# Kernel optimization log

Measured on AMD Instinct MI355X. Metric: run time of the kernel, lower is better.

The kernel has to match this reference:

```python
import jax, jax.numpy as jnp
import numpy as np
import math

H = 1024      # hidden_size
NH = 16       # num_attention_heads
HD = H // NH  # head_dim = 64
FF = 4096     # intermediate_size
AD = 256      # adapter_hidden_size
NB = 320      # num_buckets
MAXD = 800    # max_bucket_distance
B = 4
S = 1024
EPS = 1e-5


def _rel_bucket(rel):
    # HF WavLM _relative_positions_bucket
    nb = NB // 2
    buckets = (rel > 0).astype(jnp.int32) * nb
    rel = jnp.abs(rel)
    max_exact = nb // 2
    is_small = rel < max_exact
    large = max_exact + (
        jnp.log(jnp.maximum(rel, 1).astype(jnp.float32) / max_exact)
        / math.log(MAXD / max_exact) * (nb - max_exact)
    ).astype(jnp.int32)
    large = jnp.minimum(large, nb - 1)
    return buckets + jnp.where(is_small, rel, large)


def _ln(x, g, b):
    m = x.mean(-1, keepdims=True)
    v = ((x - m) ** 2).mean(-1, keepdims=True)
    return (x - m) * jax.lax.rsqrt(v + EPS) * g + b


def setup_inputs() -> dict:
    key = jax.random.key(0)
    ks = jax.random.split(key, 12)
    sc = 0.02
    w = lambda k, shape: jax.random.normal(k, shape, jnp.float32) * sc
    return dict(
        x=jax.random.normal(ks[0], (B, S, H), jnp.float32),
        Wq=w(ks[1], (H, H)), bq=jnp.zeros((H,), jnp.float32),
        Wk=w(ks[2], (H, H)), bk=jnp.zeros((H,), jnp.float32),
        Wv=w(ks[3], (H, H)), bv=jnp.zeros((H,), jnp.float32),
        Wo=w(ks[4], (H, H)), bo=jnp.zeros((H,), jnp.float32),
        Wg=w(ks[5], (8, HD)), bg=jnp.zeros((8,), jnp.float32),
        gru_const=jnp.ones((1, NH, 1, 1), jnp.float32),
        rel_embed=w(ks[6], (NB, NH)),
        ln1_g=jnp.ones((H,), jnp.float32), ln1_b=jnp.zeros((H,), jnp.float32),
        W1=w(ks[7], (FF, H)), b1=jnp.zeros((FF,), jnp.float32),
        W2=w(ks[8], (H, FF)), b2=jnp.zeros((H,), jnp.float32),
        ln2_g=jnp.ones((H,), jnp.float32), ln2_b=jnp.zeros((H,), jnp.float32),
        Wad=w(ks[9], (AD, H)), bad=jnp.zeros((AD,), jnp.float32),
        Wau=w(ks[10], (H, AD)), bau=jnp.zeros((H,), jnp.float32),
    )


def reference(x, Wq, bq, Wk, bk, Wv, bv, Wo, bo, Wg, bg, gru_const, rel_embed,
              ln1_g, ln1_b, W1, b1, W2, b2, ln2_g, ln2_b, Wad, bad, Wau, bau):
    b, s, _ = x.shape
    # --- relative position bias (first layer: position_bias=None) ---
    pos = jnp.arange(s)
    rel = pos[None, :] - pos[:, None]                 # memory - context
    pos_bias = rel_embed[_rel_bucket(rel)].transpose(2, 0, 1)  # (nh, s, s)

    # --- GRU-style gating of the bias (per batch, head, query pos) ---
    xh = x.reshape(b, s, NH, HD).transpose(0, 2, 1, 3)         # (b, nh, s, hd)
    gproj = jnp.einsum('bhsd,ed->bhse', xh, Wg) + bg           # (b, nh, s, 8)
    gproj = gproj.reshape(b, NH, s, 2, 4).sum(-1)              # (b, nh, s, 2)
    gate = jax.nn.sigmoid(gproj)
    gate_a, gate_b = gate[..., 0:1], gate[..., 1:2]            # (b, nh, s, 1)
    gate_out = gate_a * (gate_b * gru_const - 1.0) + 2.0       # (b, nh, s, 1)
    gated_bias = gate_out * pos_bias[None]                     # (b, nh, s, s)

    # --- multi-head self-attention with additive gated bias ---
    q = (x @ Wq.T + bq).reshape(b, s, NH, HD)
    k = (x @ Wk.T + bk).reshape(b, s, NH, HD)
    v = (x @ Wv.T + bv).reshape(b, s, NH, HD)
    scores = jnp.einsum('bihd,bjhd->bhij', q, k) * (HD ** -0.5) + gated_bias
    attn = jax.nn.softmax(scores, axis=-1)
    ctx = jnp.einsum('bhij,bjhd->bihd', attn, v).reshape(b, s, H)
    attn_out = ctx @ Wo.T + bo

    # --- residual + LN, FFN + adapter (idx_without_adapter=None path) + LN ---
    h = _ln(x + attn_out, ln1_g, ln1_b)
    ff = jax.nn.gelu(h @ W1.T + b1, approximate=False) @ W2.T + b2
    adapt = jax.nn.elu(h @ Wad.T + bad) @ Wau.T + bau
    h = h + ff + adapt
    return _ln(h, ln2_g, ln2_b)
```

## Files before the change

### kernel.cpp

```cpp
#include <hip/hip_runtime.h>
#include <cmath>

typedef unsigned short u16;
using short8 = __attribute__((ext_vector_type(8))) short;
using f32x4  = __attribute__((ext_vector_type(4))) float;

__device__ __forceinline__ u16 f2bf(float f) {
  union { float f; unsigned u; } c; c.f = f;
  unsigned r = c.u + 0x7fffu + ((c.u >> 16) & 1u);
  return (u16)(r >> 16);
}
__device__ __forceinline__ float bf2f(u16 b) {
  union { unsigned u; float f; } c; c.u = ((unsigned)b) << 16;
  return c.f;
}

__device__ __forceinline__ void gld_lds16(void* lds, const void* g) {
  __builtin_amdgcn_global_load_lds(
      (const __attribute__((address_space(1))) void*)g,
      (__attribute__((address_space(3))) void*)lds, 16, 0, 0);
}

__device__ __forceinline__ float gelu_fast(float t) {
  float u = 0.7978845608f * t * (1.f + 0.044715f * t * t);
  float th = 1.f - 2.f / (__expf(2.f * u) + 1.f);
  return 0.5f * t * (1.f + th);
}

__global__ __launch_bounds__(256) void cvt_bf16(const float* __restrict__ in,
                                                u16* __restrict__ out, int n4) {
  int i = blockIdx.x * 256 + threadIdx.x;
  if (i >= n4) return;
  float4 v = ((const float4*)in)[i];
  ushort4 o;
  o.x = f2bf(v.x); o.y = f2bf(v.y); o.z = f2bf(v.z); o.w = f2bf(v.w);
  ((ushort4*)out)[i] = o;
}

__global__ __launch_bounds__(256) void cvt_pad(const float* __restrict__ in,
                                               u16* __restrict__ out,
                                               int incols4, int outstride, int n4) {
  int i = blockIdx.x * 256 + threadIdx.x;
  if (i >= n4) return;
  int row = i / incols4, c = i - row * incols4;
  float4 v = ((const float4*)in)[i];
  ushort4 o;
  o.x = f2bf(v.x); o.y = f2bf(v.y); o.z = f2bf(v.z); o.w = f2bf(v.w);
  *(ushort4*)&out[(size_t)row * outstride + c * 4] = o;
}

__global__ __launch_bounds__(256) void btab_kernel(const float* __restrict__ rel_embed,
                                                   float* __restrict__ btab) {
  int idx = blockIdx.x * 256 + threadIdx.x;
  if (idx >= 16 * 2048) return;
  int h = idx >> 11;
  int d = idx & 2047;
  if (d >= 2047) return;
  int rel = d - 1023;
  int bucket = (rel > 0) ? 160 : 0;
  int ar = rel < 0 ? -rel : rel;
  if (ar < 80) {
    bucket += ar;
  } else {
    int large = 80 + (int)(logf((float)ar / 80.0f) / 2.3025851f * 80.0f);
    if (large > 159) large = 159;
    bucket += large;
  }
  btab[h * 2048 + d] = rel_embed[bucket * 16 + h];
}

__global__ __launch_bounds__(256) void gate_kernel(const float* __restrict__ x,
                                                   const float* __restrict__ Wg,
                                                   const float* __restrict__ bg,
                                                   const float* __restrict__ gc,
                                                   float* __restrict__ gate_out) {
  int gw = blockIdx.x * 4 + (threadIdx.x >> 6);
  int lane = threadIdx.x & 63;
  int s = gw & 1023, bh = gw >> 10, b = bh >> 4, h = bh & 15;
  float wA = Wg[lane] + Wg[64 + lane] + Wg[128 + lane] + Wg[192 + lane];
  float wB = Wg[256 + lane] + Wg[320 + lane] + Wg[384 + lane] + Wg[448 + lane];
  float xv = x[((size_t)(b * 1024 + s)) * 1024 + h * 64 + lane];
  float pa = xv * wA, pb = xv * wB;
  #pragma unroll
  for (int m = 1; m < 64; m <<= 1) {
    pa += __shfl_xor(pa, m, 64);
    pb += __shfl_xor(pb, m, 64);
  }
  if (lane == 0) {
    float bgA = bg[0] + bg[1] + bg[2] + bg[3];
    float bgB = bg[4] + bg[5] + bg[6] + bg[7];
    float ga = 1.f / (1.f + expf(-(pa + bgA)));
    float gb = 1.f / (1.f + expf(-(pb + bgB)));
    gate_out[(size_t)bh * 1024 + s] = ga * (gb * gc[h] - 1.f) + 2.f;
  }
}

__global__ __launch_bounds__(256) void vtrans_kernel(const u16* __restrict__ vb,
                                                     u16* __restrict__ vt) {
  __shared__ u16 tile[64 * 65];
  int bh = blockIdx.y, b = bh >> 4, h = bh & 15;
  int s0 = blockIdx.x * 64;
  int tid = threadIdx.x;
  int r = tid >> 3, c = (tid & 7) * 8;
  #pragma unroll
  for (int p = 0; p < 2; ++p) {
    int s = p * 32 + r;
    uint4 vv = *(const uint4*)&vb[((size_t)(b * 1024 + s0 + s)) * 1024 + h * 64 + c];
    const u16* pv = (const u16*)&vv;
    #pragma unroll
    for (int e = 0; e < 8; ++e) tile[(c + e) * 65 + s] = pv[e];
  }
  __syncthreads();
  int d = tid & 63, jc0 = tid >> 6;
  #pragma unroll
  for (int jc = jc0; jc < 8; jc += 4) {
    u16 tmp[8];
    #pragma unroll
    for (int e = 0; e < 8; ++e) tmp[e] = tile[d * 65 + jc * 8 + e];
    *(uint4*)&vt[((size_t)(bh * 64 + d)) * 1024 + s0 + jc * 8] = *(uint4*)tmp;
  }
}

#define VMCNT(n) asm volatile("s_waitcnt vmcnt(" #n ")" ::: "memory")

#define G256_LDA(BUF, KK, MH)                                               \
  af_[0] = *(const short8*)&lds[BUF][0][KK][aBase + (MH) * 2048 + 0];       \
  af_[1] = *(const short8*)&lds[BUF][0][KK][aBase + (MH) * 2048 + 512];     \
  af_[2] = *(const short8*)&lds[BUF][0][KK][aBase + (MH) * 2048 + 1024];    \
  af_[3] = *(const short8*)&lds[BUF][0][KK][aBase + (MH) * 2048 + 1536];
#define G256_LDB(BUF, KK)                                                   \
  bf_[0] = *(const short8*)&lds[BUF][1][KK][bBase + 0];                     \
  bf_[1] = *(const short8*)&lds[BUF][1][KK][bBase + 512];                   \
  bf_[2] = *(const short8*)&lds[BUF][1][KK][bBase + 1024];                  \
  bf_[3] = *(const short8*)&lds[BUF][1][KK][bBase + 1536];
#define G256_MFMA(MH)                                                       \
  _Pragma("unroll") for (int mi = 0; mi < 4; ++mi)                          \
  _Pragma("unroll") for (int ni = 0; ni < 4; ++ni)                          \
    acc[(MH) * 4 + mi][ni] = __builtin_amdgcn_mfma_f32_16x16x32_bf16(       \
        af_[mi], bf_[ni], acc[(MH) * 4 + mi][ni], 0, 0, 0);
#define G256_TILE(BUF)                                                      \
  G256_LDB(BUF, 0)                                                          \
  G256_LDA(BUF, 0, 0)                                                       \
  G256_MFMA(0)                                                              \
  G256_LDA(BUF, 0, 1)                                                       \
  G256_MFMA(1)                                                              \
  G256_LDB(BUF, 1)                                                          \
  G256_LDA(BUF, 1, 0)                                                       \
  G256_MFMA(0)                                                              \
  G256_LDA(BUF, 1, 1)                                                       \
  G256_MFMA(1)

template <int MODE>
__global__ __launch_bounds__(512, 2) void gemm256(
    const u16* __restrict__ A, const u16* __restrict__ Bw,
    int lda, int ldb, int kt_hi, int kt_lo, int z_hi,
    const float* __restrict__ bias0, const float* __restrict__ bias1,
    const float* __restrict__ bias2,
    float* __restrict__ outf, float* __restrict__ outf2,
    float* __restrict__ outf3, int ldo,
    u16* __restrict__ ob0, u16* __restrict__ ob1, u16* __restrict__ ob2) {
  __shared__ __align__(16) u16 lds[2][2][2][8192];

  const int tid = threadIdx.x;
  const int lane = tid & 63, wave = tid >> 6;
  const int quad = lane >> 4, l16 = lane & 15;
  const int wm = wave >> 2, wn = wave & 3;

  const int gx = gridDim.x, gy = gridDim.y;
  int flat = blockIdx.x + gx * (blockIdx.y + gy * blockIdx.z);
  const int cpx = (gx * gy * gridDim.z) >> 3;
  flat = (flat & 7) * cpx + (flat >> 3);
  const int bmi = flat % gx;
  int rest = flat / gx;
  const int bni = rest % gy;
  const int kz = rest / gy;

  const int bm = bmi * 256, bn = bni * 256;
  const int nkt = (kz < z_hi) ? kt_hi : kt_lo;
  const int ktb = (kz < z_hi) ? kz * kt_hi : z_hi * kt_hi + (kz - z_hi) * kt_lo;

  const int srow = wave * 16 + (lane >> 2);
  const int sk = (((lane & 3) ^ ((lane >> 3) & 3)) << 3);
  const u16* aG = A + (size_t)(bm + srow) * lda + (size_t)ktb * 64 + sk;
  const u16* bG = Bw + (size_t)(bn + srow) * ldb + (size_t)ktb * 64 + sk;
  const size_t aS = (size_t)128 * lda, bS = (size_t)128 * ldb;

  const int xsw = ((quad ^ ((l16 >> 1) & 3)) << 3);
  const int aBase = (wm * 128 + l16) * 32 + xsw;
  const int bBase = (wn * 64 + l16) * 32 + xsw;

  auto stA = [&](int buf, int kh, int kt) {
    const u16* g = aG + kt * 64 + kh * 32;
    u16* d = (u16*)&lds[buf][0][kh][wave * 512];
    gld_lds16(d, g);
    gld_lds16(d + 4096, g + aS);
  };
  auto stB = [&](int buf, int kh, int kt) {
    const u16* g = bG + kt * 64 + kh * 32;
    u16* d = (u16*)&lds[buf][1][kh][wave * 512];
    gld_lds16(d, g);
    gld_lds16(d + 4096, g + bS);
  };

  f32x4 acc[8][4] = {};
  short8 af_[4], bf_[4];

  stA(0, 0, 0); stB(0, 0, 0); stA(0, 1, 0); stB(0, 1, 0);
  VMCNT(0);
  __builtin_amdgcn_s_barrier();

  for (int J = 0; J < (nkt >> 1); ++J) {
    {
      const int t1 = 2 * J + 1;
      stA(1, 0, t1); stB(1, 0, t1); stA(1, 1, t1); stB(1, 1, t1);
      G256_TILE(0)
      VMCNT(0);
      __builtin_amdgcn_s_barrier();
    }
    {
      const int t2 = 2 * J + 2;
      if (t2 < nkt) { stA(0, 0, t2); stB(0, 0, t2); stA(0, 1, t2); stB(0, 1, t2); }
      G256_TILE(1)
      VMCNT(0);
      __builtin_amdgcn_s_barrier();
    }
  }

  const int m0 = bm + wm * 128 + quad * 4;
  const int n0 = bn + wn * 64 + l16;

  if constexpr (MODE == 0) {
    const int seg = bn >> 10;
    const float* bs = seg == 0 ? bias0 : (seg == 1 ? bias1 : bias2);
    u16* dst = seg == 0 ? ob0 : (seg == 1 ? ob1 : ob2);
    const float sc = seg == 0 ? 0.125f : 1.0f;
    const int nb = (bn & 1023) + wn * 64 + l16;
    #pragma unroll
    for (int a = 0; a < 8; ++a)
      #pragma unroll
      for (int ni = 0; ni < 4; ++ni) {
        int nn = nb + ni * 16;
        float bv = bs[nn];
        #pragma unroll
        for (int r = 0; r < 4; ++r) {
          int m = m0 + a * 16 + r;
          dst[(size_t)m * 1024 + nn] = f2bf((acc[a][ni][r] + bv) * sc);
        }
      }
  } else if constexpr (MODE == 2) {
    const bool is_gelu = (bn < 4096);
    #pragma unroll
    for (int a = 0; a < 8; ++a)
      #pragma unroll
      for (int ni = 0; ni < 4; ++ni) {
        int nn = n0 + ni * 16;
        float bv = is_gelu ? bias0[nn] : bias1[nn - 4096];
        #pragma unroll
        for (int r = 0; r < 4; ++r) {
          int m = m0 + a * 16 + r;
          float t = acc[a][ni][r] + bv;
          float res;
          if (is_gelu) res = gelu_fast(t);
          else         res = t > 0.f ? t : (__expf(t) - 1.f);
          ob0[(size_t)m * 4352 + nn] = f2bf(res);
        }
      }
  } else {
    float* op = (kz == 0) ? outf
              : (kz == 1) ? outf + 4194304
              : (kz == 2) ? outf2 : outf3;
    #pragma unroll
    for (int a = 0; a < 8; ++a)
      #pragma unroll
      for (int ni = 0; ni < 4; ++ni) {
        int nn = n0 + ni * 16;
        #pragma unroll
        for (int r = 0; r < 4; ++r)
          op[(size_t)(m0 + a * 16 + r) * ldo + nn] = acc[a][ni][r];
      }
  }
}

__global__ __launch_bounds__(256, 2) void attn_kernel(
    const u16* __restrict__ qb, const u16* __restrict__ kb, const u16* __restrict__ vt,
    const float* __restrict__ gate, const float* __restrict__ btab,
    u16* __restrict__ ctxb) {
  __shared__ __align__(16) u16 Ps[4][16 * 64];
  __shared__ u16 btl[2048];
  __shared__ float gbuf[64];

  const int tid = threadIdx.x;
  const int lane = tid & 63, wave = tid >> 6;
  const int quad = lane >> 4, l16 = lane & 15;
  const int bh = blockIdx.x, b = bh >> 4, h = bh & 15;
  const int it0 = blockIdx.y * 64;

  for (int idx = tid; idx < 2047; idx += 256) btl[idx] = f2bf(btab[h * 2048 + idx]);
  if (tid < 64) gbuf[tid] = gate[(size_t)bh * 1024 + it0 + tid];

  short8 aq[2];
  #pragma unroll
  for (int c = 0; c < 2; ++c)
    aq[c] = *(const short8*)&qb[((size_t)(b * 1024 + it0 + wave * 16 + l16)) * 1024 +
                                h * 64 + c * 32 + quad * 8];

  short8 kA[2][4], kB[2][4];
  auto loadK = [&](short8 (&kr)[2][4], int jt) {
    const int j0 = jt * 64;
    #pragma unroll
    for (int c = 0; c < 2; ++c)
      #pragma unroll
      for (int nt = 0; nt < 4; ++nt)
        kr[c][nt] = *(const short8*)&kb[((size_t)(b * 1024 + j0 + nt * 16 + l16)) * 1024 +
                                        h * 64 + c * 32 + quad * 8];
  };
  loadK(kA, 0);

  f32x4 oacc[4] = {};
  float mrow[4], lrow[4];
  #pragma unroll
  for (int r = 0; r < 4; ++r) { mrow[r] = -1e30f; lrow[r] = 0.f; }

  __syncthreads();

  auto body = [&](int jt, short8 (&kc)[2][4], short8 (&kn)[2][4], bool pf) {
    const int j0 = jt * 64;
    if (pf) loadK(kn, jt + 1);

    f32x4 sacc[4] = {};
    #pragma unroll
    for (int c = 0; c < 2; ++c)
      #pragma unroll
      for (int nt = 0; nt < 4; ++nt)
        sacc[nt] = __builtin_amdgcn_mfma_f32_16x16x32_bf16(aq[c], kc[c][nt], sacc[nt], 0, 0, 0);

    short8 bv[2][4];
    #pragma unroll
    for (int c = 0; c < 2; ++c)
      #pragma unroll
      for (int dt = 0; dt < 4; ++dt)
        bv[c][dt] = *(const short8*)&vt[((size_t)(bh * 64 + dt * 16 + l16)) * 1024 +
                                        j0 + c * 32 + quad * 8];

    float sc[4][4], mt[4];
    #pragma unroll
    for (int r = 0; r < 4; ++r) {
      int i_loc = wave * 16 + quad * 4 + r;
      int i_glob = it0 + i_loc;
      float g = gbuf[i_loc];
      float mx = -1e30f;
      #pragma unroll
      for (int nt = 0; nt < 4; ++nt) {
        int j = j0 + nt * 16 + l16;
        float s = sacc[nt][r] + g * bf2f(btl[j - i_glob + 1023]);
        sc[nt][r] = s;
        mx = fmaxf(mx, s);
      }
      mt[r] = mx;
    }
    #pragma unroll
    for (int m = 1; m < 16; m <<= 1)
      #pragma unroll
      for (int r = 0; r < 4; ++r) mt[r] = fmaxf(mt[r], __shfl_xor(mt[r], m, 64));

    float alpha[4], ls[4];
    #pragma unroll
    for (int r = 0; r < 4; ++r) {
      float mnew = fmaxf(mrow[r], mt[r]);
      alpha[r] = __expf(mrow[r] - mnew);
      mrow[r] = mnew;
      float lsum = 0.f;
      #pragma unroll
      for (int nt = 0; nt < 4; ++nt) {
        float p = __expf(sc[nt][r] - mnew);
        sc[nt][r] = p;
        lsum += p;
      }
      ls[r] = lsum;
    }
    #pragma unroll
    for (int m = 1; m < 16; m <<= 1)
      #pragma unroll
      for (int r = 0; r < 4; ++r) ls[r] += __shfl_xor(ls[r], m, 64);
    #pragma unroll
    for (int r = 0; r < 4; ++r) lrow[r] = lrow[r] * alpha[r] + ls[r];

    #pragma unroll
    for (int nt = 0; nt < 4; ++nt)
      #pragma unroll
      for (int r = 0; r < 4; ++r)
        Ps[wave][(nt * 2 + (l16 >> 3)) * 128 + (quad * 4 + r) * 8 + (l16 & 7)] = f2bf(sc[nt][r]);

    #pragma unroll
    for (int dt = 0; dt < 4; ++dt)
      #pragma unroll
      for (int r = 0; r < 4; ++r) oacc[dt][r] *= alpha[r];

    #pragma unroll
    for (int c = 0; c < 2; ++c) {
      short8 ap = *(const short8*)&Ps[wave][(c * 4 + quad) * 128 + l16 * 8];
      #pragma unroll
      for (int dt = 0; dt < 4; ++dt)
        oacc[dt] = __builtin_amdgcn_mfma_f32_16x16x32_bf16(ap, bv[c][dt], oacc[dt], 0, 0, 0);
    }
  };

  for (int J = 0; J < 8; ++J) {
    body(2 * J,     kA, kB, true);
    body(2 * J + 1, kB, kA, J < 7);
  }

  #pragma unroll
  for (int dt = 0; dt < 4; ++dt)
    #pragma unroll
    for (int r = 0; r < 4; ++r) {
      int i_loc = wave * 16 + quad * 4 + r;
      int d = dt * 16 + l16;
      float o = oacc[dt][r] / lrow[r];
      ctxb[((size_t)(b * 1024 + it0 + i_loc)) * 1024 + h * 64 + d] = f2bf(o);
    }
}

template <bool WRITE_BF16, bool TWO_BIAS, int NP>
__global__ __launch_bounds__(256) void redln_kernel(
    const float* __restrict__ p0, const float* __restrict__ p1,
    const float* __restrict__ p2, const float* __restrict__ p3,
    const float* __restrict__ extra, const float* __restrict__ bias,
    const float* __restrict__ bias2,
    const float* __restrict__ g, const float* __restrict__ bta,
    float* __restrict__ outf, u16* __restrict__ outb) {
  __shared__ float red[8];
  int row = blockIdx.x, tid = threadIdx.x;
  int lane = tid & 63, wave = tid >> 6;
  size_t base = (size_t)row * 1024 + tid * 4;
  float4 a = *(const float4*)&p0[base];
  float4 bb = *(const float4*)&p1[base];
  float4 c = *(const float4*)&extra[base];
  float4 d = *(const float4*)&bias[tid * 4];
  float4 v;
  v.x = a.x + bb.x + c.x + d.x;
  v.y = a.y + bb.y + c.y + d.y;
  v.z = a.z + bb.z + c.z + d.z;
  v.w = a.w + bb.w + c.w + d.w;
  if (NP == 4) {
    float4 e2 = *(const float4*)&p2[base];
    float4 e3 = *(const float4*)&p3[base];
    v.x += e2.x + e3.x; v.y += e2.y + e3.y;
    v.z += e2.z + e3.z; v.w += e2.w + e3.w;
  }
  if (TWO_BIAS) {
    float4 d2 = *(const float4*)&bias2[tid * 4];
    v.x += d2.x; v.y += d2.y; v.z += d2.z; v.w += d2.w;
  }
  float s = v.x + v.y + v.z + v.w;
  #pragma unroll
  for (int m = 1; m < 64; m <<= 1) s += __shfl_xor(s, m, 64);
  if (lane == 0) red[wave] = s;
  __syncthreads();
  float mean = (red[0] + red[1] + red[2] + red[3]) * (1.f / 1024.f);
  float d0 = v.x - mean, d1 = v.y - mean, d2 = v.z - mean, d3 = v.w - mean;
  float sq = d0 * d0 + d1 * d1 + d2 * d2 + d3 * d3;
  #pragma unroll
  for (int m = 1; m < 64; m <<= 1) sq += __shfl_xor(sq, m, 64);
  if (lane == 0) red[4 + wave] = sq;
  __syncthreads();
  float var = (red[4] + red[5] + red[6] + red[7]) * (1.f / 1024.f);
  float rstd = rsqrtf(var + 1e-5f);
  float dd[4] = {d0, d1, d2, d3};
  #pragma unroll
  for (int e = 0; e < 4; ++e) {
    int cidx = tid * 4 + e;
    float val = dd[e] * rstd * g[cidx] + bta[cidx];
    outf[(size_t)row * 1024 + cidx] = val;
    if (WRITE_BF16) outb[(size_t)row * 1024 + cidx] = f2bf(val);
  }
}

extern "C" void kernel_launch(void* const* d_in, const int* in_sizes, int n_in,
                              void* d_out, int out_size, void* d_ws, size_t ws_size,
                              hipStream_t stream) {
  const float* x    = (const float*)d_in[0];
  const float* Wq   = (const float*)d_in[1];  const float* bq  = (const float*)d_in[2];
  const float* Wk   = (const float*)d_in[3];  const float* bk  = (const float*)d_in[4];
  const float* Wv   = (const float*)d_in[5];  const float* bv  = (const float*)d_in[6];
  const float* Wo   = (const float*)d_in[7];  const float* bo  = (const float*)d_in[8];
  const float* Wg   = (const float*)d_in[9];  const float* bg  = (const float*)d_in[10];
  const float* gc   = (const float*)d_in[11];
  const float* rel  = (const float*)d_in[12];
  const float* ln1g = (const float*)d_in[13]; const float* ln1b = (const float*)d_in[14];
  const float* W1   = (const float*)d_in[15]; const float* b1  = (const float*)d_in[16];
  const float* W2   = (const float*)d_in[17]; const float* b2  = (const float*)d_in[18];
  const float* ln2g = (const float*)d_in[19]; const float* ln2b = (const float*)d_in[20];
  const float* Wad  = (const float*)d_in[21]; const float* bad = (const float*)d_in[22];
  const float* Wau  = (const float*)d_in[23]; const float* bau = (const float*)d_in[24];
  float* out = (float*)d_out;

  char* ws = (char*)d_ws;
  const size_t MB = 1ull << 20;
  const size_t KB = 1ull << 10;
  (void)n_in; (void)in_sizes; (void)out_size;

  const bool big = ws_size >= (135ull << 20);

  u16 *xb, *wqkv, *qb, *kb, *vbp, *vtb, *ctxb, *wob, *w1ad, *w2au, *ffadp, *hb;
  float *gate, *btab, *P0, *P1, *P2, *P3, *hf;
  xb    = (u16*)(ws + 0 * MB);
  wqkv  = (u16*)(ws + 8 * MB);
  ffadp = (u16*)(ws + 0 * MB);
  P0    = (float*)(ws + 34 * MB);
  P1    = (float*)(ws + 50 * MB);
  float* PW2 = (float*)(ws + 0 * MB);
  float* PW3 = (float*)(ws + 16 * MB);
  if (big) {
    P2   = (float*)(ws + 66 * MB);
    P3   = (float*)(ws + 82 * MB);
    qb   = (u16*)(ws + 66 * MB);
    kb   = (u16*)(ws + 74 * MB);
    vbp  = (u16*)(ws + 82 * MB);
    vtb  = (u16*)(ws + 90 * MB);
    hb   = (u16*)(ws + 82 * MB);
    ctxb = (u16*)(ws + 98 * MB);
    hf   = (float*)(ws + 98 * MB);
    wob  = (u16*)(ws + 114 * MB);
    w1ad = (u16*)(ws + 116 * MB);
    w2au = (u16*)(ws + 125 * MB);
    gate = (float*)(ws + 133 * MB + 512 * KB);
    btab = (float*)(ws + 133 * MB + 768 * KB);
  } else {
    qb   = (u16*)(ws + 14 * MB);
    kb   = (u16*)(ws + 22 * MB);
    vbp  = (u16*)(ws + 30 * MB);
    vtb  = (u16*)(ws + 38 * MB);
    gate = (float*)(ws + 46 * MB);
    btab = (float*)(ws + 46 * MB + 256 * KB);
    ctxb = (u16*)(ws + 66 * MB);
    wob  = (u16*)(ws + 74 * MB);
    w1ad = (u16*)(ws + 76 * MB);
    w2au = (u16*)(ws + 85 * MB);
    hf   = (float*)(ws + 94 * MB);
    hb   = (u16*)(ws + 110 * MB);
    P2   = (float*)(ws + 66 * MB);
    P3   = (float*)(ws + 14 * MB);
  }

  auto cvt = [&](const float* src, u16* dst, int n) {
    cvt_bf16<<<(n / 4 + 255) / 256, 256, 0, stream>>>(src, dst, n / 4);
  };
  cvt(x, xb, 4096 * 1024);
  cvt(Wq, wqkv,               1024 * 1024);
  cvt(Wk, wqkv + 1024 * 1024, 1024 * 1024);
  cvt(Wv, wqkv + 2 * 1024 * 1024, 1024 * 1024);
  cvt(Wo, wob, 1024 * 1024);
  cvt(W1, w1ad, 4096 * 1024);
  cvt(Wad, w1ad + 4096 * 1024, 256 * 1024);
  cvt_pad<<<(1024 * 1024 + 255) / 256, 256, 0, stream>>>(W2, w2au, 1024, 4352, 1024 * 1024);
  cvt_pad<<<(64 * 1024 + 255) / 256, 256, 0, stream>>>(Wau, w2au + 4096, 64, 4352, 64 * 1024);

  btab_kernel<<<128, 256, 0, stream>>>(rel, btab);
  gate_kernel<<<16384, 256, 0, stream>>>(x, Wg, bg, gc, gate);

  gemm256<0><<<dim3(16, 12, 1), 512, 0, stream>>>(xb, wqkv, 1024, 1024, 16, 16, 1,
      bq, bk, bv, nullptr, nullptr, nullptr, 0, qb, kb, vbp);
  vtrans_kernel<<<dim3(16, 64), 256, 0, stream>>>(vbp, vtb);
  attn_kernel<<<dim3(64, 16), 256, 0, stream>>>(qb, kb, vtb, gate, btab, ctxb);
  gemm256<3><<<dim3(16, 4, 4), 512, 0, stream>>>(ctxb, wob, 1024, 1024, 4, 4, 4,
      nullptr, nullptr, nullptr, P0, PW2, PW3, 1024, nullptr, nullptr, nullptr);
  redln_kernel<true, false, 4><<<4096, 256, 0, stream>>>(P0, P1, PW2, PW3, x, bo, nullptr,
      ln1g, ln1b, hf, hb);
  gemm256<2><<<dim3(16, 17, 1), 512, 0, stream>>>(hb, w1ad, 1024, 1024, 16, 16, 1,
      b1, bad, nullptr, nullptr, nullptr, nullptr, 0, ffadp, nullptr, nullptr);
  gemm256<3><<<dim3(16, 4, 4), 512, 0, stream>>>(ffadp, w2au, 4352, 4352, 18, 16, 2,
      nullptr, nullptr, nullptr, P0, P2, P3, 1024, nullptr, nullptr, nullptr);
  redln_kernel<false, true, 4><<<4096, 256, 0, stream>>>(P0, P1, P2, P3, hf, b2, bau,
      ln2g, ln2b, out, nullptr);
}
```

Baseline: 531.5 us.

## Stage K/V tiles in double-buffered LDS via direct global-to-LDS loads

The attention kernel now has the four waves cooperatively copy each 64x64 K and V tile into double-buffered shared memory with global_load_lds. Each wave then reads its MFMA operands from LDS instead of loading full K and V tiles from global memory separately. This removes the fourfold redundant global traffic for K/V across waves, at the cost of a workgroup barrier every iteration and more LDS use. The occupancy hint of 2 blocks per CU is dropped.

```diff
diff --git a/kernel.cpp b/kernel.cpp
--- a/kernel.cpp
+++ b/kernel.cpp
@@ -281,10 +281,12 @@
   }
 }
 
-__global__ __launch_bounds__(256, 2) void attn_kernel(
+__global__ __launch_bounds__(256) void attn_kernel(
     const u16* __restrict__ qb, const u16* __restrict__ kb, const u16* __restrict__ vt,
     const float* __restrict__ gate, const float* __restrict__ btab,
     u16* __restrict__ ctxb) {
+  __shared__ __align__(16) u16 Ks[2][64 * 64];
+  __shared__ __align__(16) u16 Vs[2][64 * 64];
   __shared__ __align__(16) u16 Ps[4][16 * 64];
   __shared__ u16 btl[2048];
   __shared__ float gbuf[64];
@@ -294,6 +296,19 @@
   const int quad = lane >> 4, l16 = lane & 15;
   const int bh = blockIdx.x, b = bh >> 4, h = bh & 15;
   const int it0 = blockIdx.y * 64;
+  const int sr = lane & 15;
+  const int skc = (lane >> 4) * 8;
+
+  auto stage = [&](int buf, int jt) {
+    const int j0 = jt * 64;
+    #pragma unroll
+    for (int hf = 0; hf < 2; ++hf) {
+      gld_lds16(&Ks[buf][wave * 1024 + hf * 512],
+                &kb[((size_t)(b * 1024 + j0 + wave * 16 + sr)) * 1024 + h * 64 + hf * 32 + skc]);
+      gld_lds16(&Vs[buf][wave * 1024 + hf * 512],
+                &vt[((size_t)(bh * 64 + wave * 16 + sr)) * 1024 + j0 + hf * 32 + skc]);
+    }
+  };
 
   for (int idx = tid; idx < 2047; idx += 256) btl[idx] = f2bf(btab[h * 2048 + idx]);
   if (tid < 64) gbuf[tid] = gate[(size_t)bh * 1024 + it0 + tid];
@@ -304,43 +319,28 @@
     aq[c] = *(const short8*)&qb[((size_t)(b * 1024 + it0 + wave * 16 + l16)) * 1024 +
                                 h * 64 + c * 32 + quad * 8];
 
-  short8 kA[2][4], kB[2][4];
-  auto loadK = [&](short8 (&kr)[2][4], int jt) {
-    const int j0 = jt * 64;
-    #pragma unroll
-    for (int c = 0; c < 2; ++c)
-      #pragma unroll
-      for (int nt = 0; nt < 4; ++nt)
-        kr[c][nt] = *(const short8*)&kb[((size_t)(b * 1024 + j0 + nt * 16 + l16)) * 1024 +
-                                        h * 64 + c * 32 + quad * 8];
-  };
-  loadK(kA, 0);
-
   f32x4 oacc[4] = {};
   float mrow[4], lrow[4];
   #pragma unroll
   for (int r = 0; r < 4; ++r) { mrow[r] = -1e30f; lrow[r] = 0.f; }
 
+  stage(0, 0);
   __syncthreads();
 
-  auto body = [&](int jt, short8 (&kc)[2][4], short8 (&kn)[2][4], bool pf) {
+  for (int jt = 0; jt < 16; ++jt) {
+    const int cur = jt & 1;
     const int j0 = jt * 64;
-    if (pf) loadK(kn, jt + 1);
+    if (jt < 15) stage(cur ^ 1, jt + 1);
 
     f32x4 sacc[4] = {};
     #pragma unroll
-    for (int c = 0; c < 2; ++c)
-      #pragma unroll
-      for (int nt = 0; nt < 4; ++nt)
-        sacc[nt] = __builtin_amdgcn_mfma_f32_16x16x32_bf16(aq[c], kc[c][nt], sacc[nt], 0, 0, 0);
-
-    short8 bv[2][4];
-    #pragma unroll
-    for (int c = 0; c < 2; ++c)
-      #pragma unroll
-      for (int dt = 0; dt < 4; ++dt)
-        bv[c][dt] = *(const short8*)&vt[((size_t)(bh * 64 + dt * 16 + l16)) * 1024 +
-                                        j0 + c * 32 + quad * 8];
+    for (int c = 0; c < 2; ++c) {
+      #pragma unroll
+      for (int nt = 0; nt < 4; ++nt) {
+        short8 bk8 = *(const short8*)&Ks[cur][nt * 1024 + (c * 4 + quad) * 128 + l16 * 8];
+        sacc[nt] = __builtin_amdgcn_mfma_f32_16x16x32_bf16(aq[c], bk8, sacc[nt], 0, 0, 0);
+      }
+    }
 
     float sc[4][4], mt[4];
     #pragma unroll
@@ -400,14 +400,14 @@
     for (int c = 0; c < 2; ++c) {
       short8 ap = *(const short8*)&Ps[wave][(c * 4 + quad) * 128 + l16 * 8];
       #pragma unroll
-      for (int dt = 0; dt < 4; ++dt)
-        oacc[dt] = __builtin_amdgcn_mfma_f32_16x16x32_bf16(ap, bv[c][dt], oacc[dt], 0, 0, 0);
-    }
-  };
-
-  for (int J = 0; J < 8; ++J) {
-    body(2 * J,     kA, kB, true);
-    body(2 * J + 1, kB, kA, J < 7);
+      for (int dt = 0; dt < 4; ++dt) {
+        short8 bv8 = *(const short8*)&Vs[cur][dt * 1024 + (c * 4 + quad) * 128 + l16 * 8];
+        oacc[dt] = __builtin_amdgcn_mfma_f32_16x16x32_bf16(ap, bv8, oacc[dt], 0, 0, 0);
+      }
+    }
+
+    VMCNT(0);
+    __builtin_amdgcn_s_barrier();
   }
 
   #pragma unroll
```

Result: faster. 488.1 us (-8.2%).
